# Performance work log

Hardware: AMD Instinct MI355X
Metric: run time of the kernel (lower is better)

Reference implementation:

```python
import jax, jax.numpy as jnp
import numpy as np

B = 32
M = 3
MAG_DIM = 20
STD = 0.28
INV = float(1.0 / (np.sqrt(2.0) * STD))
NORM = float(1.0 / (np.sqrt(2.0 * np.pi) * STD))


def _lrelu(x):
    return jax.nn.leaky_relu(x, 0.01)


def _conv(x, w, b):
    y = jax.lax.conv_general_dilated(x, w, (2, 2), 'VALID',
                                     dimension_numbers=('NCHW', 'OIHW', 'NCHW'))
    return _lrelu(y + b[None, :, None, None])


def _combos(x):
    # x: [N, c, d] -> [N, c, c, 2d], pairs[n, i, j] = concat(x[n, i], x[n, j])
    # (matches torch getCombinations: tensorB = expand-over-i, tensorA = expand-over-j)
    N, c, d = x.shape
    left = jnp.broadcast_to(x[:, :, None, :], (N, c, c, d))
    right = jnp.broadcast_to(x[:, None, :, :], (N, c, c, d))
    return jnp.concatenate([left, right], axis=-1)


def _forward(batch, conv_w1, conv_b1, conv_w2, conv_b2, conv_w3, conv_b3, conv_w4, conv_b4,
             post_w, post_b, g_w1, g_b1, g_w2, g_b2, g_w3, g_b3, g_w4, g_b4,
             h_w1, h_b1, h_w2, h_b2, h_w3, h_b3, f_w1, f_b1, f_w2, f_b2, ff_w, ff_b):
    bsz = batch.shape[0]
    x = batch.reshape(bsz * 16, 1, 80, 80)
    # magnitude encoding (computed under no_grad in the original)
    mag = jnp.linspace(-1.0, 1.0, MAG_DIM).astype(batch.dtype)  # [20]
    t = jnp.tanh(x * (2.0 / 255.0) - 1.0)                        # [N,1,80,80]
    enc = NORM * jnp.exp(-(((t + mag[None, :, None, None]) * INV) ** 2))  # [N,20,80,80]
    enc = jax.lax.stop_gradient(enc)
    y = _conv(enc, conv_w1, conv_b1)   # [N,32,39,39]
    y = _conv(y, conv_w2, conv_b2)     # [N,32,19,19]
    y = _conv(y, conv_w3, conv_b3)     # [N,32,9,9]
    y = _conv(y, conv_w4, conv_b4)     # [N,32,4,4]
    obj = y.reshape(bsz * 16, 512) @ post_w + post_b             # [N,247]
    panel = obj.reshape(bsz, 16, 247)
    given, options = panel[:, :8], panel[:, 8:]
    giv = jnp.broadcast_to(given[:, None], (bsz, 8, 8, 247))
    ctx = jnp.concatenate([giv, options[:, :, None, :]], axis=2)  # [B,8,9,247]
    tags = jnp.broadcast_to(jnp.eye(9, dtype=batch.dtype), (bsz * 8, 9, 9))
    objects = jnp.concatenate([ctx.reshape(bsz * 8, 9, 247), tags], axis=-1)  # [B*8,9,256]

    z = _combos(objects).reshape(-1, 512)  # [B*8*81, 512]
    z = _lrelu(z @ g_w1 + g_b1)
    z = _lrelu(z @ g_w2 + g_b2)
    z = _lrelu(z @ g_w3 + g_b3)
    z = _lrelu(z @ g_w4 + g_b4)
    sum_j = z.reshape(bsz * 8, 9, 9, 256).sum(axis=2)  # [B*8,9,256]
    for i in range(h_w1.shape[0]):
        p = _combos(sum_j).reshape(-1, 512)
        z = _lrelu(p @ h_w1[i] + h_b1[i])
        z = _lrelu(z @ h_w2[i] + h_b2[i])
        z = _lrelu(z @ h_w3[i] + h_b3[i])
        sum_j = z.reshape(bsz * 8, 9, 9, 256).sum(axis=2)
    h_sum = sum_j.sum(axis=1)                          # [B*8,256]
    z = _lrelu(h_sum @ f_w1 + f_b1)
    z = _lrelu(z @ f_w2 + f_b2)
    result = z @ ff_w + ff_b                           # [B*8,1]
    answer = result.reshape(bsz, 8)
    loss = jnp.mean(h_sum ** 2) + jnp.mean(result ** 2)
    return answer, loss


def setup_inputs():
    key = jax.random.key(0)
    ks = iter(jax.random.split(key, 40))

    def U(shape, fan_in):
        s = 1.0 / np.sqrt(fan_in)
        return jax.random.uniform(next(ks), shape, jnp.float32, -s, s)

    inp = {
        'batch': jax.random.uniform(next(ks), (B, 16, 80, 80), jnp.float32, 0.0, 255.0),
        'conv_w1': U((32, MAG_DIM, 3, 3), MAG_DIM * 9), 'conv_b1': U((32,), MAG_DIM * 9),
        'conv_w2': U((32, 32, 3, 3), 288), 'conv_b2': U((32,), 288),
        'conv_w3': U((32, 32, 3, 3), 288), 'conv_b3': U((32,), 288),
        'conv_w4': U((32, 32, 3, 3), 288), 'conv_b4': U((32,), 288),
        'post_w': U((512, 247), 512), 'post_b': U((247,), 512),
        'g_w1': U((512, 512), 512), 'g_b1': U((512,), 512),
        'g_w2': U((512, 512), 512), 'g_b2': U((512,), 512),
        'g_w3': U((512, 512), 512), 'g_b3': U((512,), 512),
        'g_w4': U((512, 256), 512), 'g_b4': U((256,), 512),
        'h_w1': U((M, 512, 256), 512), 'h_b1': U((M, 256), 512),
        'h_w2': U((M, 256, 256), 256), 'h_b2': U((M, 256), 256),
        'h_w3': U((M, 256, 256), 256), 'h_b3': U((M, 256), 256),
        'f_w1': U((256, 256), 256), 'f_b1': U((256,), 256),
        'f_w2': U((256, 256), 256), 'f_b2': U((256,), 256),
        'ff_w': U((256, 1), 256), 'ff_b': U((1,), 256),
    }
    return inp


def reference(batch, conv_w1, conv_b1, conv_w2, conv_b2, conv_w3, conv_b3, conv_w4, conv_b4,
              post_w, post_b, g_w1, g_b1, g_w2, g_b2, g_w3, g_b3, g_w4, g_b4,
              h_w1, h_b1, h_w2, h_b2, h_w3, h_b3, f_w1, f_b1, f_w2, f_b2, ff_w, ff_b):
    return _forward(batch, conv_w1, conv_b1, conv_w2, conv_b2, conv_w3, conv_b3, conv_w4, conv_b4,
                    post_w, post_b, g_w1, g_b1, g_w2, g_b2, g_w3, g_b3, g_w4, g_b4,
                    h_w1, h_b1, h_w2, h_b2, h_w3, h_b3, f_w1, f_b1, f_w2, f_b2, ff_w, ff_b)
```

## Files before the change

### kernel.cpp

```cpp
#include <hip/hip_runtime.h>
#include <hip/hip_bf16.h>
#include <math.h>

static __device__ __forceinline__ float lrelu(float v){ return v > 0.0f ? v : 0.01f*v; }

static __device__ __forceinline__ unsigned short f2bf(float f){
  unsigned int u = __float_as_uint(f);
  unsigned int r = (u + 0x7fffu + ((u >> 16) & 1u)) >> 16;
  return (unsigned short)r;
}
static __device__ __forceinline__ float bf2f(unsigned short u){
  return __uint_as_float(((unsigned int)u) << 16);
}
static __device__ __forceinline__ unsigned int pack_bf2(float lo, float hi){
  __hip_bfloat162 bb = __float22bfloat162_rn(make_float2(lo, hi));
  return *reinterpret_cast<unsigned int*>(&bb);
}

#define ENC_INV  2.5253813613805277f
#define ENC_NORM 1.4247939f

typedef __attribute__((ext_vector_type(4))) float f32x4;
typedef __attribute__((ext_vector_type(8))) short bf16x8;

__global__ __launch_bounds__(256) void k_prep(
    const float* __restrict__ g_w1, const float* __restrict__ g_w2,
    const float* __restrict__ g_w3, const float* __restrict__ g_w4,
    const float* __restrict__ h_w1, const float* __restrict__ h_w2,
    const float* __restrict__ h_w3, const float* __restrict__ post_w,
    const float* __restrict__ conv_w2, const float* __restrict__ conv_w3,
    const float* __restrict__ conv_w4, const float* __restrict__ conv_w1,
    const float* __restrict__ f_w1, const float* __restrict__ f_w2,
    unsigned short* __restrict__ WT)
{
  int e = blockIdx.x*256 + threadIdx.x;
  float v;
  if (e < 262144) {
    int nn = e >> 8, kk = e & 255;
    v = (nn < 512) ? g_w1[kk*512 + nn] : g_w1[(256+kk)*512 + (nn-512)];
  } else if (e < 524288) {
    int r = e - 262144; int nn = r >> 9, kk = r & 511;
    v = g_w2[kk*512 + nn];
  } else if (e < 786432) {
    int r = e - 524288; int nn = r >> 9, kk = r & 511;
    v = g_w3[kk*512 + nn];
  } else if (e < 917504) {
    int r = e - 786432; int nn = r >> 9, kk = r & 511;
    v = g_w4[kk*256 + nn];
  } else if (e < 1310720) {
    int r = e - 917504; int i = r >> 17; int q = r & 131071;
    int nn = q >> 8, kk = q & 255;
    v = (nn < 256) ? h_w1[i*131072 + kk*256 + nn]
                   : h_w1[i*131072 + (256+kk)*256 + (nn-256)];
  } else if (e < 1507328) {
    int r = e - 1310720; int i = r >> 16; int q = r & 65535;
    int nn = q >> 8, kk = q & 255;
    v = h_w2[i*65536 + kk*256 + nn];
  } else if (e < 1703936) {
    int r = e - 1507328; int i = r >> 16; int q = r & 65535;
    int nn = q >> 8, kk = q & 255;
    v = h_w3[i*65536 + kk*256 + nn];
  } else if (e < 1835008) {
    int r = e - 1703936; int np = r >> 9, kp = r & 511;
    int px = kp >> 5, c = kp & 31;
    v = (np < 247) ? post_w[(c*16+px)*247 + np] : 0.f;
  } else if (e < 1862656) {
    int r = e - 1835008; int which = r / 9216; int q = r % 9216;
    int tap = q >> 10, o = (q >> 5) & 31, c = q & 31;
    const float* w = which==0 ? conv_w2 : (which==1 ? conv_w3 : conv_w4);
    v = w[(o*32+c)*9 + tap];
  } else if (e < 1871872) {
    int r = e - 1862656; int tap = r >> 10, o = (r >> 5) & 31, c = r & 31;
    v = (c < 20) ? conv_w1[(o*20+c)*9 + tap] : 0.f;
  } else if (e < 1937408) {
    int r = e - 1871872; int nn = r >> 8, kk = r & 255;
    v = f_w1[kk*256 + nn];
  } else {
    int r = e - 1937408; int nn = r >> 8, kk = r & 255;
    v = f_w2[kk*256 + nn];
  }
  WT[e] = f2bf(v);
}

__global__ __launch_bounds__(256) void k_conv1m(
    const float* __restrict__ batch, const unsigned short* __restrict__ wc1,
    const float* __restrict__ bias, unsigned short* __restrict__ y)
{
  __shared__ unsigned short ench[7][80][40];
  int n = blockIdx.x;
  int orow0 = blockIdx.y * 3;
  int irow0 = orow0 * 2;
  int tid = threadIdx.x;
  int lane = tid & 63, wid = tid >> 6;
  int lr = lane & 15, kg = lane >> 4;

  bf16x8 bf0[9], bf1[9];
  #pragma unroll
  for (int tap = 0; tap < 9; ++tap) {
    bf0[tap] = *(const bf16x8*)&wc1[tap*1024 + lr*32 + kg*8];
    bf1[tap] = *(const bf16x8*)&wc1[tap*1024 + (16+lr)*32 + kg*8];
  }

  const float* img = batch + (size_t)n*6400 + irow0*80;
  for (int p = tid; p < 7*79; p += 256) {
    int r = p / 79, col = p % 79;
    float x = img[r*80 + col];
    float t = tanhf(x * (2.0f/255.0f) - 1.0f);
    unsigned int pk[16];
    #pragma unroll
    for (int cp = 0; cp < 10; ++cp) {
      float mg0 = -1.0f + (2.0f/19.0f)*(float)(2*cp);
      float mg1 = -1.0f + (2.0f/19.0f)*(float)(2*cp+1);
      float u0 = (t + mg0)*ENC_INV, u1 = (t + mg1)*ENC_INV;
      pk[cp] = pack_bf2(ENC_NORM*__expf(-u0*u0), ENC_NORM*__expf(-u1*u1));
    }
    #pragma unroll
    for (int cp = 10; cp < 16; ++cp) pk[cp] = 0u;
    int hidx = (col & 1) ? 40 + (col >> 1) : (col >> 1);
    unsigned short* dst = &ench[r][hidx][0];
    *(uint4*)(dst)      = *(uint4*)&pk[0];
    *(uint4*)(dst + 8)  = *(uint4*)&pk[4];
    *(uint4*)(dst + 16) = *(uint4*)&pk[8];
    *(uint4*)(dst + 24) = *(uint4*)&pk[12];
  }
  __syncthreads();

  const int totpx = 117;
  float b0 = bias[lr], b1 = bias[16 + lr];
  for (int t = wid; t < 8; t += 4) {
    int pa = t*16 + lr;
    int pc = (pa < totpx) ? pa : (totpx - 1);
    int oh = pc / 39, ow = pc % 39;
    f32x4 acc0 = {0.f,0.f,0.f,0.f}, acc1 = {0.f,0.f,0.f,0.f};
    #pragma unroll
    for (int kh = 0; kh < 3; ++kh) {
      int r = oh*2 + kh;
      #pragma unroll
      for (int kw = 0; kw < 3; ++kw) {
        int hidx = (kw == 1) ? (40 + ow) : (ow + (kw >> 1));
        bf16x8 a = *(const bf16x8*)&ench[r][hidx][kg*8];
        int tap = kh*3 + kw;
        acc0 = __builtin_amdgcn_mfma_f32_16x16x32_bf16(a, bf0[tap], acc0, 0, 0, 0);
        acc1 = __builtin_amdgcn_mfma_f32_16x16x32_bf16(a, bf1[tap], acc1, 0, 0, 0);
      }
    }
    #pragma unroll
    for (int rr = 0; rr < 4; ++rr) {
      int ps = t*16 + kg*4 + rr;
      if (ps < totpx) {
        int soh = orow0 + ps / 39, sow = ps % 39;
        unsigned short* op = y + (((size_t)n*39 + soh)*39 + sow)*32;
        op[lr]      = f2bf(lrelu(acc0[rr] + b0));
        op[16 + lr] = f2bf(lrelu(acc1[rr] + b1));
      }
    }
  }
}

template<int H, int W, int OH, int OW, int ROWS>
__global__ __launch_bounds__(256) void k_cmfma(
    const unsigned short* __restrict__ in, const unsigned short* __restrict__ wc,
    const float* __restrict__ bias, unsigned short* __restrict__ out)
{
  constexpr int IR = 2*ROWS + 1;
  __shared__ unsigned short xs[IR][W][40];
  int n = blockIdx.x;
  int orow0 = blockIdx.y * ROWS;
  int nrows = min(ROWS, OH - orow0);
  int irow0 = orow0 * 2;
  int ir = min(2*nrows + 1, H - irow0);
  int tid = threadIdx.x;
  int lane = tid & 63, wid = tid >> 6;
  int lr = lane & 15, kg = lane >> 4;

  bf16x8 bf0[9], bf1[9];
  #pragma unroll
  for (int tap = 0; tap < 9; ++tap) {
    bf0[tap] = *(const bf16x8*)&wc[(tap*32 + lr)*32      + kg*8];
    bf1[tap] = *(const bf16x8*)&wc[(tap*32 + 16 + lr)*32 + kg*8];
  }

  const unsigned short* ip = in + ((size_t)n*H + irow0)*W*32;
  int npx = ir * W;
  for (int p = tid; p < npx; p += 256) {
    const uint4* src = (const uint4*)(ip + (size_t)p*32);
    uint4 v0 = src[0], v1 = src[1], v2 = src[2], v3 = src[3];
    int r = p / W, col = p % W;
    unsigned short* dst = &xs[r][col][0];
    *(uint4*)(dst)      = v0;
    *(uint4*)(dst + 8)  = v1;
    *(uint4*)(dst + 16) = v2;
    *(uint4*)(dst + 24) = v3;
  }
  __syncthreads();

  int totpx = nrows * OW;
  int ntiles = (totpx + 15) >> 4;
  float b0 = bias[lr], b1 = bias[16 + lr];
  for (int t = wid; t < ntiles; t += 4) {
    int pa = t*16 + lr;
    int pc = (pa < totpx) ? pa : 0;
    int oh = pc / OW, ow = pc % OW;
    f32x4 acc0 = {0.f,0.f,0.f,0.f}, acc1 = {0.f,0.f,0.f,0.f};
    #pragma unroll
    for (int kh = 0; kh < 3; ++kh)
      #pragma unroll
      for (int kw = 0; kw < 3; ++kw) {
        bf16x8 a = *(const bf16x8*)&xs[oh*2 + kh][ow*2 + kw][kg*8];
        acc0 = __builtin_amdgcn_mfma_f32_16x16x32_bf16(a, bf0[kh*3+kw], acc0, 0, 0, 0);
        acc1 = __builtin_amdgcn_mfma_f32_16x16x32_bf16(a, bf1[kh*3+kw], acc1, 0, 0, 0);
      }
    #pragma unroll
    for (int rr = 0; rr < 4; ++rr) {
      int ps = t*16 + kg*4 + rr;
      if (ps < totpx) {
        int soh = orow0 + ps / OW, sow = ps % OW;
        unsigned short* op = out + (((size_t)n*OH + soh)*OW + sow)*32;
        op[lr]      = f2bf(lrelu(acc0[rr] + b0));
        op[16 + lr] = f2bf(lrelu(acc1[rr] + b1));
      }
    }
  }
}

template<int OUT_BF16, int ACT>
__global__ __launch_bounds__(256) void k_mgemm(
    const unsigned short* __restrict__ A, const unsigned short* __restrict__ Wt,
    const float* __restrict__ bias, void* __restrict__ Cv,
    int M, int N, int K)
{
  __shared__ unsigned short As[128][72];
  __shared__ unsigned short Bs[128][72];
  int bm = blockIdx.x * 128;
  int bn = blockIdx.y * 128;
  int tid = threadIdx.x;
  int wid = tid >> 6, lane = tid & 63;
  int wr = (wid >> 1) * 64, wc = (wid & 1) * 64;
  int lr = lane & 15, lk = (lane >> 4) * 8;

  f32x4 acc[4][4];
  #pragma unroll
  for (int i = 0; i < 4; ++i)
    #pragma unroll
    for (int j = 0; j < 4; ++j)
      acc[i][j] = (f32x4){0.f,0.f,0.f,0.f};

  for (int k0 = 0; k0 < K; k0 += 64) {
    #pragma unroll
    for (int i = 0; i < 4; ++i) {
      int ch = tid + (i << 8);
      int r = ch >> 3, kc = (ch & 7) * 8;
      *(uint4*)&As[r][kc] = *(const uint4*)&A[(size_t)(bm + r)*K + k0 + kc];
      *(uint4*)&Bs[r][kc] = *(const uint4*)&Wt[(size_t)(bn + r)*K + k0 + kc];
    }
    __syncthreads();
    #pragma unroll
    for (int ks = 0; ks < 2; ++ks) {
      bf16x8 a[4], b[4];
      #pragma unroll
      for (int i = 0; i < 4; ++i)
        a[i] = *(const bf16x8*)&As[wr + i*16 + lr][ks*32 + lk];
      #pragma unroll
      for (int i = 0; i < 4; ++i)
        b[i] = *(const bf16x8*)&Bs[wc + i*16 + lr][ks*32 + lk];
      #pragma unroll
      for (int i = 0; i < 4; ++i)
        #pragma unroll
        for (int j = 0; j < 4; ++j)
          acc[i][j] = __builtin_amdgcn_mfma_f32_16x16x32_bf16(a[i], b[j], acc[i][j], 0, 0, 0);
    }
    __syncthreads();
  }
  int r0 = (lane >> 4) * 4;
  #pragma unroll
  for (int i = 0; i < 4; ++i) {
    #pragma unroll
    for (int j = 0; j < 4; ++j) {
      int col = bn + wc + j*16 + lr;
      float bv = bias ? bias[col] : 0.f;
      #pragma unroll
      for (int rr = 0; rr < 4; ++rr) {
        int row = bm + wr + i*16 + r0 + rr;
        float v = acc[i][j][rr] + bv;
        if (ACT) v = lrelu(v);
        if (OUT_BF16) ((unsigned short*)Cv)[(size_t)row*N + col] = f2bf(v);
        else          ((float*)Cv)[(size_t)row*N + col] = v;
      }
    }
  }
}

__global__ void k_objects(const float* __restrict__ panel, const float* __restrict__ post_b,
                          unsigned short* __restrict__ obj)
{
  int idx = blockIdx.x*256 + threadIdx.x;
  int row = idx >> 8;
  int k = idx & 255;
  int slot = row % 9;
  int nn = row / 9;
  int b = nn >> 3, opt = nn & 7;
  float v;
  if (k < 247) {
    int src = (slot < 8) ? (b*16 + slot) : (b*16 + 8 + opt);
    v = panel[(size_t)src*256 + k] + post_b[k];
  } else {
    v = ((k - 247) == slot) ? 1.0f : 0.0f;
  }
  obj[idx] = f2bf(v);
}

__global__ void k_expand(const unsigned short* __restrict__ UV, const float* __restrict__ bias,
                         unsigned short* __restrict__ Z, int N)
{
  int idx = blockIdx.x*256 + threadIdx.x;
  int m = idx / N, k = idx % N;
  int n = m / 81, r = m % 81;
  int i = r / 9, j = r % 9;
  int ld = 2*N;
  float v = bf2f(UV[(size_t)(n*9 + i)*ld + k]) + bf2f(UV[(size_t)(n*9 + j)*ld + N + k]) + bias[k];
  Z[idx] = f2bf(lrelu(v));
}

__global__ void k_sumj(const unsigned short* __restrict__ Z, float* __restrict__ SJ,
                       unsigned short* __restrict__ SJb, int C)
{
  int idx = blockIdx.x*256 + threadIdx.x;
  int orow = idx / C, k = idx % C;
  int n = orow / 9, i = orow % 9;
  const unsigned short* base = Z + (size_t)(n*81 + i*9)*C + k;
  float s = 0.f;
  #pragma unroll
  for (int j = 0; j < 9; ++j) s += bf2f(base[(size_t)j*C]);
  SJ[idx] = s;
  SJb[idx] = f2bf(s);
}

__global__ void k_hsum(const float* __restrict__ SJ, float* __restrict__ HS,
                       unsigned short* __restrict__ HSb)
{
  int idx = blockIdx.x*256 + threadIdx.x;
  int n = idx >> 8, k = idx & 255;
  const float* base = SJ + (size_t)n*9*256 + k;
  float s = 0.f;
  #pragma unroll
  for (int i = 0; i < 9; ++i) s += base[i*256];
  HS[idx] = s;
  HSb[idx] = f2bf(s);
}

__global__ __launch_bounds__(256) void k_tailfin(
    const float* __restrict__ HS, const unsigned short* __restrict__ F2,
    const float* __restrict__ ffw, const float* __restrict__ ffb,
    float* __restrict__ out)
{
  __shared__ float red[256];
  __shared__ float wsm[256];
  int tid = threadIdx.x;
  wsm[tid] = ffw[tid];
  float s = 0.f;
  for (int j = 0; j < 256; ++j) { float v = HS[j*256 + tid]; s += v*v; }
  red[tid] = s; __syncthreads();
  for (int off = 128; off > 0; off >>= 1) { if (tid < off) red[tid] += red[tid + off]; __syncthreads(); }
  float hsq = red[0];
  __syncthreads();
  float r = ffb[0];
  for (int k = 0; k < 256; ++k) r += bf2f(F2[(size_t)tid*256 + k])*wsm[k];
  red[tid] = r*r; __syncthreads();
  for (int off = 128; off > 0; off >>= 1) { if (tid < off) red[tid] += red[tid + off]; __syncthreads(); }
  out[tid] = r;
  if (tid == 0) out[256] = hsq/65536.0f + red[0]/256.0f;
}

extern "C" void kernel_launch(void* const* d_in, const int* in_sizes, int n_in,
                              void* d_out, int out_size, void* d_ws, size_t ws_size,
                              hipStream_t stream)
{
  const float* batch   = (const float*)d_in[0];
  const float* conv_w1 = (const float*)d_in[1];
  const float* conv_b1 = (const float*)d_in[2];
  const float* conv_w2 = (const float*)d_in[3];
  const float* conv_b2 = (const float*)d_in[4];
  const float* conv_w3 = (const float*)d_in[5];
  const float* conv_b3 = (const float*)d_in[6];
  const float* conv_w4 = (const float*)d_in[7];
  const float* conv_b4 = (const float*)d_in[8];
  const float* post_w  = (const float*)d_in[9];
  const float* post_b  = (const float*)d_in[10];
  const float* g_w1    = (const float*)d_in[11];
  const float* g_b1    = (const float*)d_in[12];
  const float* g_w2    = (const float*)d_in[13];
  const float* g_b2    = (const float*)d_in[14];
  const float* g_w3    = (const float*)d_in[15];
  const float* g_b3    = (const float*)d_in[16];
  const float* g_w4    = (const float*)d_in[17];
  const float* g_b4    = (const float*)d_in[18];
  const float* h_w1    = (const float*)d_in[19];
  const float* h_b1    = (const float*)d_in[20];
  const float* h_w2    = (const float*)d_in[21];
  const float* h_b2    = (const float*)d_in[22];
  const float* h_w3    = (const float*)d_in[23];
  const float* h_b3    = (const float*)d_in[24];
  const float* f_w1    = (const float*)d_in[25];
  const float* f_b1    = (const float*)d_in[26];
  const float* f_w2    = (const float*)d_in[27];
  const float* f_b2    = (const float*)d_in[28];
  const float* ff_w    = (const float*)d_in[29];
  const float* ff_b    = (const float*)d_in[30];

  char* wsb = (char*)d_ws;
  const size_t off_Y1    = 0;
  const size_t off_Y2    = 52000000;
  const size_t off_Y3    = 64000000;
  const size_t off_Y4    = 67000000;
  const size_t off_PANEL = 68000000;
  const size_t off_WT    = 132000000;
  const size_t off_Pb    = 0;
  const size_t off_Qb    = 22000000;
  const size_t off_UV    = 44000000;
  const size_t off_OBJb  = 54000000;
  const size_t off_SJ    = 56000000;
  const size_t off_SJb   = 59000000;
  const size_t off_HS    = 61000000;
  const size_t off_HSb   = 61500000;
  const size_t off_F1    = 62000000;
  const size_t off_F2    = 63000000;

  unsigned short* WT = (unsigned short*)(wsb + off_WT);
  const size_t wt_g1   = 0;
  const size_t wt_g2   = 262144;
  const size_t wt_g3   = 524288;
  const size_t wt_g4   = 786432;
  const size_t wt_h1   = 917504;
  const size_t wt_h2   = 1310720;
  const size_t wt_h3   = 1507328;
  const size_t wt_post = 1703936;
  const size_t wt_cw2  = 1835008;
  const size_t wt_cw3  = 1844224;
  const size_t wt_cw4  = 1853440;
  const size_t wt_cw1  = 1862656;
  const size_t wt_f1   = 1871872;
  const size_t wt_f2   = 1937408;

  dim3 b256(256);

  k_prep<<<dim3(7824), b256, 0, stream>>>(g_w1, g_w2, g_w3, g_w4, h_w1, h_w2, h_w3,
                                          post_w, conv_w2, conv_w3, conv_w4, conv_w1,
                                          f_w1, f_w2, WT);

  unsigned short* Y1 = (unsigned short*)(wsb + off_Y1);
  unsigned short* Y2 = (unsigned short*)(wsb + off_Y2);
  unsigned short* Y3 = (unsigned short*)(wsb + off_Y3);
  unsigned short* Y4 = (unsigned short*)(wsb + off_Y4);
  float* PANEL = (float*)(wsb + off_PANEL);

  k_conv1m<<<dim3(512,13), b256, 0, stream>>>(batch, WT + wt_cw1, conv_b1, Y1);
  k_cmfma<39,39,19,19,10><<<dim3(512,2), b256, 0, stream>>>(Y1, WT + wt_cw2, conv_b2, Y2);
  k_cmfma<19,19, 9, 9, 9><<<dim3(512,1), b256, 0, stream>>>(Y2, WT + wt_cw3, conv_b3, Y3);
  k_cmfma< 9, 9, 4, 4, 4><<<dim3(512,1), b256, 0, stream>>>(Y3, WT + wt_cw4, conv_b4, Y4);

  k_mgemm<0,0><<<dim3(4,2), b256, 0, stream>>>(Y4, WT + wt_post, nullptr, PANEL, 512,256,512);

  unsigned short* OBJb = (unsigned short*)(wsb + off_OBJb);
  unsigned short* Pb   = (unsigned short*)(wsb + off_Pb);
  unsigned short* Qb   = (unsigned short*)(wsb + off_Qb);
  unsigned short* SJb  = (unsigned short*)(wsb + off_SJb);
  unsigned short* UVb  = (unsigned short*)(wsb + off_UV);
  float* SJ = (float*)(wsb + off_SJ);
  float* HS = (float*)(wsb + off_HS);
  unsigned short* HSb = (unsigned short*)(wsb + off_HSb);
  unsigned short* F1 = (unsigned short*)(wsb + off_F1);
  unsigned short* F2 = (unsigned short*)(wsb + off_F2);

  k_objects<<<dim3(2304), b256, 0, stream>>>(PANEL, post_b, OBJb);

  k_mgemm<1,0><<<dim3(18,8), b256, 0, stream>>>(OBJb, WT + wt_g1, nullptr, UVb, 2304,1024,256);
  k_expand<<<dim3(20736*512/256), b256, 0, stream>>>(UVb, g_b1, Pb, 512);
  k_mgemm<1,1><<<dim3(162,4), b256, 0, stream>>>(Pb, WT + wt_g2, g_b2, Qb, 20736,512,512);
  k_mgemm<1,1><<<dim3(162,4), b256, 0, stream>>>(Qb, WT + wt_g3, g_b3, Pb, 20736,512,512);
  k_mgemm<1,1><<<dim3(162,2), b256, 0, stream>>>(Pb, WT + wt_g4, g_b4, Qb, 20736,256,512);
  k_sumj<<<dim3(2304), b256, 0, stream>>>(Qb, SJ, SJb, 256);

  for (int i = 0; i < 3; ++i) {
    k_mgemm<1,0><<<dim3(18,4), b256, 0, stream>>>(SJb, WT + wt_h1 + (size_t)i*131072, nullptr, UVb, 2304,512,256);
    k_expand<<<dim3(20736*256/256), b256, 0, stream>>>(UVb, h_b1 + i*256, Pb, 256);
    k_mgemm<1,1><<<dim3(162,2), b256, 0, stream>>>(Pb, WT + wt_h2 + (size_t)i*65536, h_b2 + i*256, Qb, 20736,256,256);
    k_mgemm<1,1><<<dim3(162,2), b256, 0, stream>>>(Qb, WT + wt_h3 + (size_t)i*65536, h_b3 + i*256, Pb, 20736,256,256);
    k_sumj<<<dim3(2304), b256, 0, stream>>>(Pb, SJ, SJb, 256);
  }

  k_hsum<<<dim3(256), b256, 0, stream>>>(SJ, HS, HSb);
  k_mgemm<1,1><<<dim3(2,2), b256, 0, stream>>>(HSb, WT + wt_f1, f_b1, F1, 256,256,256);
  k_mgemm<1,1><<<dim3(2,2), b256, 0, stream>>>(F1,  WT + wt_f2, f_b2, F2, 256,256,256);
  k_tailfin<<<dim3(1), b256, 0, stream>>>(HS, F2, ff_w, ff_b, (float*)d_out);
}
```

Before: 411.0 us.

## Fuse pair expansion into following GEMM and use Gaussian recurrence for encoding

Removes the separate expand kernels that materialised the full pairwise activation tensor. The following GEMM (k_pgemm) now builds its A tile on the fly from the U/V rows plus bias and leaky-ReLU while loading shared memory, which avoids a large write and re-read of the 20736-row intermediate. Separately, the magnitude-encoding loop replaces twenty exps with a geometric recurrence, and tanh with an exp/rcp form. The recurrence can drift slightly in precision, and the fused loader does per-element arithmetic in the GEMM load path.

```diff
diff --git a/kernel.cpp b/kernel.cpp
--- a/kernel.cpp
+++ b/kernel.cpp
@@ -17,8 +17,11 @@
   return *reinterpret_cast<unsigned int*>(&bb);
 }
 
-#define ENC_INV  2.5253813613805277f
 #define ENC_NORM 1.4247939f
+#define GC_C     6.3775511f
+#define GC_2CD   1.3426423f
+#define GC_CD2   0.070665395f
+#define GC_S1    0.86820227f
 
 typedef __attribute__((ext_vector_type(4))) float f32x4;
 typedef __attribute__((ext_vector_type(8))) short bf16x8;
@@ -102,22 +105,27 @@
   }
 
   const float* img = batch + (size_t)n*6400 + irow0*80;
+  const float S2 = GC_S1 * GC_S1;
   for (int p = tid; p < 7*79; p += 256) {
-    int r = p / 79, col = p % 79;
-    float x = img[r*80 + col];
-    float t = tanhf(x * (2.0f/255.0f) - 1.0f);
+    int row = p / 79, col = p % 79;
+    float x = img[row*80 + col];
+    float E = __expf(x * (4.0f/255.0f) - 2.0f);
+    float t = 1.0f - 2.0f*__builtin_amdgcn_rcpf(E + 1.0f);
+    float z = t - 1.0f;
+    float e = ENC_NORM * __expf(-GC_C*z*z);
+    float rg = __expf(-GC_2CD*z - GC_CD2);
     unsigned int pk[16];
     #pragma unroll
     for (int cp = 0; cp < 10; ++cp) {
-      float mg0 = -1.0f + (2.0f/19.0f)*(float)(2*cp);
-      float mg1 = -1.0f + (2.0f/19.0f)*(float)(2*cp+1);
-      float u0 = (t + mg0)*ENC_INV, u1 = (t + mg1)*ENC_INV;
-      pk[cp] = pack_bf2(ENC_NORM*__expf(-u0*u0), ENC_NORM*__expf(-u1*u1));
+      float e1 = e * rg;
+      pk[cp] = pack_bf2(e, e1);
+      e  = e1 * rg * GC_S1;
+      rg = rg * S2;
     }
     #pragma unroll
     for (int cp = 10; cp < 16; ++cp) pk[cp] = 0u;
     int hidx = (col & 1) ? 40 + (col >> 1) : (col >> 1);
-    unsigned short* dst = &ench[r][hidx][0];
+    unsigned short* dst = &ench[row][hidx][0];
     *(uint4*)(dst)      = *(uint4*)&pk[0];
     *(uint4*)(dst + 8)  = *(uint4*)&pk[4];
     *(uint4*)(dst + 16) = *(uint4*)&pk[8];
@@ -285,6 +293,95 @@
         if (ACT) v = lrelu(v);
         if (OUT_BF16) ((unsigned short*)Cv)[(size_t)row*N + col] = f2bf(v);
         else          ((float*)Cv)[(size_t)row*N + col] = v;
+      }
+    }
+  }
+}
+
+__global__ __launch_bounds__(256) void k_pgemm(
+    const unsigned short* __restrict__ UV, const unsigned short* __restrict__ Wt,
+    const float* __restrict__ abias, const float* __restrict__ obias,
+    unsigned short* __restrict__ C, int M, int N, int K)
+{
+  __shared__ unsigned short As[128][72];
+  __shared__ unsigned short Bs[128][72];
+  __shared__ float absm[512];
+  int bm = blockIdx.x * 128;
+  int bn = blockIdx.y * 128;
+  int tid = threadIdx.x;
+  int wid = tid >> 6, lane = tid & 63;
+  int wr = (wid >> 1) * 64, wc = (wid & 1) * 64;
+  int lr = lane & 15, lk = (lane >> 4) * 8;
+  int ld = 2*K;
+
+  for (int idx = tid; idx < K; idx += 256) absm[idx] = abias[idx];
+  __syncthreads();
+
+  int urow[4], vrow[4];
+  #pragma unroll
+  for (int i = 0; i < 4; ++i) {
+    int r = (tid + (i << 8)) >> 3;
+    int m = bm + r;
+    int n = m / 81; int rem = m - n*81;
+    int ii = rem / 9; int jj = rem - ii*9;
+    urow[i] = n*9 + ii; vrow[i] = n*9 + jj;
+  }
+
+  f32x4 acc[4][4];
+  #pragma unroll
+  for (int i = 0; i < 4; ++i)
+    #pragma unroll
+    for (int j = 0; j < 4; ++j)
+      acc[i][j] = (f32x4){0.f,0.f,0.f,0.f};
+
+  for (int k0 = 0; k0 < K; k0 += 64) {
+    #pragma unroll
+    for (int i = 0; i < 4; ++i) {
+      int ch = tid + (i << 8);
+      int r = ch >> 3, kc = (ch & 7) * 8;
+      uint4 u4 = *(const uint4*)&UV[(size_t)urow[i]*ld + k0 + kc];
+      uint4 v4 = *(const uint4*)&UV[(size_t)vrow[i]*ld + K + k0 + kc];
+      const unsigned short* us = (const unsigned short*)&u4;
+      const unsigned short* vs = (const unsigned short*)&v4;
+      unsigned int pk[4];
+      #pragma unroll
+      for (int e2 = 0; e2 < 4; ++e2) {
+        float a0 = bf2f(us[2*e2])   + bf2f(vs[2*e2])   + absm[k0 + kc + 2*e2];
+        float a1 = bf2f(us[2*e2+1]) + bf2f(vs[2*e2+1]) + absm[k0 + kc + 2*e2+1];
+        pk[e2] = pack_bf2(lrelu(a0), lrelu(a1));
+      }
+      *(uint4*)&As[r][kc] = *(uint4*)pk;
+      *(uint4*)&Bs[r][kc] = *(const uint4*)&Wt[(size_t)(bn + r)*K + k0 + kc];
+    }
+    __syncthreads();
+    #pragma unroll
+    for (int ks = 0; ks < 2; ++ks) {
+      bf16x8 a[4], b[4];
+      #pragma unroll
+      for (int i = 0; i < 4; ++i)
+        a[i] = *(const bf16x8*)&As[wr + i*16 + lr][ks*32 + lk];
+      #pragma unroll
+      for (int i = 0; i < 4; ++i)
+        b[i] = *(const bf16x8*)&Bs[wc + i*16 + lr][ks*32 + lk];
+      #pragma unroll
+      for (int i = 0; i < 4; ++i)
+        #pragma unroll
+        for (int j = 0; j < 4; ++j)
+          acc[i][j] = __builtin_amdgcn_mfma_f32_16x16x32_bf16(a[i], b[j], acc[i][j], 0, 0, 0);
+    }
+    __syncthreads();
+  }
+  int r0 = (lane >> 4) * 4;
+  #pragma unroll
+  for (int i = 0; i < 4; ++i) {
+    #pragma unroll
+    for (int j = 0; j < 4; ++j) {
+      int col = bn + wc + j*16 + lr;
+      float bv = obias[col];
+      #pragma unroll
+      for (int rr = 0; rr < 4; ++rr) {
+        int row = bm + wr + i*16 + r0 + rr;
+        C[(size_t)row*N + col] = f2bf(lrelu(acc[i][j][rr] + bv));
       }
     }
   }
@@ -307,18 +404,6 @@
     v = ((k - 247) == slot) ? 1.0f : 0.0f;
   }
   obj[idx] = f2bf(v);
-}
-
-__global__ void k_expand(const unsigned short* __restrict__ UV, const float* __restrict__ bias,
-                         unsigned short* __restrict__ Z, int N)
-{
-  int idx = blockIdx.x*256 + threadIdx.x;
-  int m = idx / N, k = idx % N;
-  int n = m / 81, r = m % 81;
-  int i = r / 9, j = r % 9;
-  int ld = 2*N;
-  float v = bf2f(UV[(size_t)(n*9 + i)*ld + k]) + bf2f(UV[(size_t)(n*9 + j)*ld + N + k]) + bias[k];
-  Z[idx] = f2bf(lrelu(v));
 }
 
 __global__ void k_sumj(const unsigned short* __restrict__ Z, float* __restrict__ SJ,
@@ -474,16 +559,14 @@
   k_objects<<<dim3(2304), b256, 0, stream>>>(PANEL, post_b, OBJb);
 
   k_mgemm<1,0><<<dim3(18,8), b256, 0, stream>>>(OBJb, WT + wt_g1, nullptr, UVb, 2304,1024,256);
-  k_expand<<<dim3(20736*512/256), b256, 0, stream>>>(UVb, g_b1, Pb, 512);
-  k_mgemm<1,1><<<dim3(162,4), b256, 0, stream>>>(Pb, WT + wt_g2, g_b2, Qb, 20736,512,512);
+  k_pgemm<<<dim3(162,4), b256, 0, stream>>>(UVb, WT + wt_g2, g_b1, g_b2, Qb, 20736,512,512);
   k_mgemm<1,1><<<dim3(162,4), b256, 0, stream>>>(Qb, WT + wt_g3, g_b3, Pb, 20736,512,512);
   k_mgemm<1,1><<<dim3(162,2), b256, 0, stream>>>(Pb, WT + wt_g4, g_b4, Qb, 20736,256,512);
   k_sumj<<<dim3(2304), b256, 0, stream>>>(Qb, SJ, SJb, 256);
 
   for (int i = 0; i < 3; ++i) {
     k_mgemm<1,0><<<dim3(18,4), b256, 0, stream>>>(SJb, WT + wt_h1 + (size_t)i*131072, nullptr, UVb, 2304,512,256);
-    k_expand<<<dim3(20736*256/256), b256, 0, stream>>>(UVb, h_b1 + i*256, Pb, 256);
-    k_mgemm<1,1><<<dim3(162,2), b256, 0, stream>>>(Pb, WT + wt_h2 + (size_t)i*65536, h_b2 + i*256, Qb, 20736,256,256);
+    k_pgemm<<<dim3(162,2), b256, 0, stream>>>(UVb, WT + wt_h2 + (size_t)i*65536, h_b1 + i*256, h_b2 + i*256, Qb, 20736,256,256);
     k_mgemm<1,1><<<dim3(162,2), b256, 0, stream>>>(Qb, WT + wt_h3 + (size_t)i*65536, h_b3 + i*256, Pb, 20736,256,256);
     k_sumj<<<dim3(2304), b256, 0, stream>>>(Pb, SJ, SJb, 256);
   }
```

Result: faster. 363.5 us (-11.6%).
